# Kernel tuning notes

Hardware: AMD Instinct MI355X
Metric: run time of the kernel (lower is better)

The kernel has to match this reference:

```python
import jax, jax.numpy as jnp
import numpy as np

EPS = 1e-5
NUM_GROUPS = 8


def setup_inputs() -> dict:
    key = jax.random.key(0)
    ks = jax.random.split(key, 8)
    B, C, H, W = 4, 64, 64, 64
    scale_w = 1.0 / np.sqrt(C)  # roughly xavier scale for [C,C]
    return {
        "x": jax.random.normal(ks[0], (B, C, H, W), dtype=jnp.float32),
        "gamma": jnp.ones((C,), dtype=jnp.float32),
        "beta": jnp.zeros((C,), dtype=jnp.float32),
        "Wq": jax.random.normal(ks[1], (C, C), dtype=jnp.float32) * scale_w,
        "bq": jnp.zeros((C,), dtype=jnp.float32),
        "Wk": jax.random.normal(ks[2], (C, C), dtype=jnp.float32) * scale_w,
        "bk": jnp.zeros((C,), dtype=jnp.float32),
        "Wv": jax.random.normal(ks[3], (C, C), dtype=jnp.float32) * scale_w,
        "bv": jnp.zeros((C,), dtype=jnp.float32),
        "Wp": jax.random.normal(ks[4], (C, C), dtype=jnp.float32) * scale_w,
        "bp": jnp.zeros((C,), dtype=jnp.float32),
    }


def _group_norm(x, gamma, beta):
    # x: [B, C, H, W]; normalize over (C//G, H, W) within each of G groups
    B, C, H, W = x.shape
    xg = x.reshape(B, NUM_GROUPS, -1)
    mean = jnp.mean(xg, axis=-1, keepdims=True)
    var = jnp.var(xg, axis=-1, keepdims=True)
    xn = ((xg - mean) * jax.lax.rsqrt(var + EPS)).reshape(B, C, H, W)
    return xn * gamma[None, :, None, None] + beta[None, :, None, None]


def reference(x, gamma, beta, Wq, bq, Wk, bk, Wv, bv, Wp, bp):
    B, C, H, W = x.shape
    N = H * W
    xn = _group_norm(x, gamma, beta).reshape(B, C, N)  # [B, C, N]
    # 1x1 convs == per-pixel linear maps over channels
    q = jnp.einsum('oc,bcn->bon', Wq, xn) + bq[None, :, None]  # [B, C, N]
    k = jnp.einsum('oc,bcn->bon', Wk, xn) + bk[None, :, None]
    v = jnp.einsum('oc,bcn->bon', Wv, xn) + bv[None, :, None]
    scale = 1.0 / jnp.sqrt(jnp.asarray(C, dtype=x.dtype))
    attn = jnp.einsum('bcn,bcm->bnm', q, k) * scale  # [B, N, N]
    attn = jax.nn.softmax(attn, axis=-1)
    out = jnp.einsum('bnm,bcm->bcn', attn, v)  # [B, C, N]
    out = jnp.einsum('oc,bcn->bon', Wp, out) + bp[None, :, None]
    return x + out.reshape(B, C, H, W)
```

## Files before the change

kernel.cpp:

```cpp
#include <hip/hip_runtime.h>
#include <math.h>

#define B_ 4
#define C_ 64
#define N_ 4096

typedef unsigned short u16;
typedef __attribute__((ext_vector_type(8))) short bf16x8;
typedef __attribute__((ext_vector_type(4))) float f32x4;
typedef __attribute__((ext_vector_type(16))) float f32x16;
typedef __attribute__((ext_vector_type(2))) int i32x2;

__device__ __forceinline__ u16 f2bf(float f) {
    unsigned u = __float_as_uint(f);
    u += 0x7fff + ((u >> 16) & 1);
    return (u16)(u >> 16);
}
__device__ __forceinline__ float bf2f(u16 h) {
    return __uint_as_float(((unsigned)h) << 16);
}

__global__ __launch_bounds__(256) void gn_reduce(const float* __restrict__ x,
                                                 float* __restrict__ partials) {
    int bg = blockIdx.x >> 3, chunk = blockIdx.x & 7;
    const float4* xv = (const float4*)(x + (size_t)bg * 32768 + (size_t)chunk * 4096);
    float s = 0.f, ss = 0.f;
    #pragma unroll
    for (int k = 0; k < 4; k++) {
        float4 v = xv[threadIdx.x + 256 * k];
        s += v.x + v.y + v.z + v.w;
        ss += v.x * v.x + v.y * v.y + v.z * v.z + v.w * v.w;
    }
    #pragma unroll
    for (int off = 1; off < 64; off <<= 1) {
        s += __shfl_xor(s, off);
        ss += __shfl_xor(ss, off);
    }
    __shared__ float red[2][4];
    int w = threadIdx.x >> 6;
    if ((threadIdx.x & 63) == 0) { red[0][w] = s; red[1][w] = ss; }
    __syncthreads();
    if (threadIdx.x == 0) {
        s = red[0][0] + red[0][1] + red[0][2] + red[0][3];
        ss = red[1][0] + red[1][1] + red[1][2] + red[1][3];
        partials[bg * 16 + chunk * 2] = s;
        partials[bg * 16 + chunk * 2 + 1] = ss;
    }
}

__global__ __launch_bounds__(256) void qkv_kernel(
    const float* __restrict__ x, const float* __restrict__ gamma,
    const float* __restrict__ beta, const float* __restrict__ partials,
    const float* __restrict__ Wq, const float* __restrict__ bq,
    const float* __restrict__ Wk, const float* __restrict__ bk,
    const float* __restrict__ Wv, const float* __restrict__ bv,
    u16* __restrict__ Qo, u16* __restrict__ Ko, u16* __restrict__ Vt) {
    __shared__ __align__(16) u16 wt[3][64][64];
    __shared__ __align__(16) u16 xs[64][64];
    __shared__ __align__(16) u16 odt[64][72];

    const int b = blockIdx.x >> 6;
    const int nt = blockIdx.x & 63;
    const int tid = threadIdx.x;
    const float* Ws[3] = {Wq, Wk, Wv};
    const float* bs[3] = {bq, bk, bv};

    {
        const int rw = tid >> 2, qd = tid & 3;
        #pragma unroll
        for (int s = 0; s < 3; s++) {
            const float4* wsrc = (const float4*)(Ws[s] + rw * 64 + qd * 16);
            float4 f0 = wsrc[0], f1 = wsrc[1], f2 = wsrc[2], f3 = wsrc[3];
            u16 pk[16];
            pk[0]=f2bf(f0.x); pk[1]=f2bf(f0.y); pk[2]=f2bf(f0.z); pk[3]=f2bf(f0.w);
            pk[4]=f2bf(f1.x); pk[5]=f2bf(f1.y); pk[6]=f2bf(f1.z); pk[7]=f2bf(f1.w);
            pk[8]=f2bf(f2.x); pk[9]=f2bf(f2.y); pk[10]=f2bf(f2.z); pk[11]=f2bf(f2.w);
            pk[12]=f2bf(f3.x); pk[13]=f2bf(f3.y); pk[14]=f2bf(f3.z); pk[15]=f2bf(f3.w);
            int blk0 = (2 * qd) ^ (rw & 7), blk1 = (2 * qd + 1) ^ (rw & 7);
            *(uint4*)&wt[s][rw][blk0 * 8] = *(uint4*)&pk[0];
            *(uint4*)&wt[s][rw][blk1 * 8] = *(uint4*)&pk[8];
        }
    }
    {
        const int c = tid >> 2, px0 = (tid & 3) * 16;
        const int g = c >> 3, bg = b * 8 + g;
        float s = 0.f, ss = 0.f;
        #pragma unroll
        for (int i = 0; i < 8; i++) {
            s += partials[bg * 16 + i * 2];
            ss += partials[bg * 16 + i * 2 + 1];
        }
        float mean = s * (1.f / 32768.f);
        float var = ss * (1.f / 32768.f) - mean * mean;
        float rstd = rsqrtf(var + 1e-5f);
        float ga = gamma[c] * rstd;
        float bb = beta[c] - mean * ga;
        const float4* xp = (const float4*)(x + ((size_t)(b * 64 + c)) * N_ + nt * 64 + px0);
        float4 q0 = xp[0], q1 = xp[1], q2 = xp[2], q3 = xp[3];
        float vals[16] = {q0.x,q0.y,q0.z,q0.w, q1.x,q1.y,q1.z,q1.w,
                          q2.x,q2.y,q2.z,q2.w, q3.x,q3.y,q3.z,q3.w};
        #pragma unroll
        for (int e = 0; e < 16; e++) {
            int px = px0 + e;
            xs[px][((c >> 3) ^ (px & 7)) * 8 + (c & 7)] = f2bf(vals[e] * ga + bb);
        }
    }
    __syncthreads();

    const int lane = tid & 63, w = tid >> 6;
    const int lr = lane & 15, lg = lane >> 4;
    const f32x4 zz = {0.f, 0.f, 0.f, 0.f};
    const int sa0 = (lg ^ (lr & 7)) * 8, sa1 = ((4 | lg) ^ (lr & 7)) * 8;

    #pragma unroll
    for (int s = 0; s < 3; s++) {
        bf16x8 a0 = *(const bf16x8*)&wt[s][w * 16 + lr][sa0];
        bf16x8 a1 = *(const bf16x8*)&wt[s][w * 16 + lr][sa1];
        float bias[4];
        #pragma unroll
        for (int r = 0; r < 4; r++) bias[r] = bs[s][w * 16 + lg * 4 + r];
        #pragma unroll
        for (int pt = 0; pt < 4; pt++) {
            bf16x8 b0 = *(const bf16x8*)&xs[pt * 16 + lr][sa0];
            bf16x8 b1 = *(const bf16x8*)&xs[pt * 16 + lr][sa1];
            f32x4 acc = __builtin_amdgcn_mfma_f32_16x16x32_bf16(a0, b0, zz, 0, 0, 0);
            acc = __builtin_amdgcn_mfma_f32_16x16x32_bf16(a1, b1, acc, 0, 0, 0);
            if (s == 0) {
                #pragma unroll
                for (int r = 0; r < 4; r++)
                    odt[pt * 16 + lr][w * 16 + lg * 4 + r] = f2bf((acc[r] + bias[r]) * 0.18033688f);
            } else if (s == 1) {
                #pragma unroll
                for (int r = 0; r < 4; r++)
                    odt[pt * 16 + lr][w * 16 + lg * 4 + r] = f2bf(acc[r] + bias[r]);
            } else {
                #pragma unroll
                for (int r = 0; r < 4; r++)
                    odt[w * 16 + lg * 4 + r][pt * 16 + lr] = f2bf(acc[r] + bias[r]);
            }
        }
        __syncthreads();
        if (s < 2) {
            u16* dst = (s == 0 ? Qo : Ko) + ((size_t)(b * N_ + nt * 64)) * 64;
            #pragma unroll
            for (int k2 = 0; k2 < 2; k2++) {
                int c = tid + k2 * 256;
                int px = c >> 3, blk = c & 7;
                *(uint4*)(dst + (size_t)px * 64 + blk * 8) = *(const uint4*)&odt[px][blk * 8];
            }
        } else {
            #pragma unroll
            for (int k2 = 0; k2 < 2; k2++) {
                int c = tid + k2 * 256;
                int co = c >> 3, blk = c & 7;
                *(uint4*)(Vt + ((size_t)(b * 64 + co)) * N_ + nt * 64 + blk * 8) =
                    *(const uint4*)&odt[co][blk * 8];
            }
        }
        __syncthreads();
    }
}

__global__ __launch_bounds__(256, 4) void flash_kernel(
    const u16* __restrict__ Qg, const u16* __restrict__ Kg,
    const u16* __restrict__ Vg, u16* __restrict__ Opart, float* __restrict__ ml,
    int nsplit) {
    __shared__ __align__(16) u16 smem[16384];
    u16* const Ksb0 = smem;
    u16* const Ksb1 = smem + 4096;
    u16* const Vsb0 = smem + 8192;
    u16* const Vsb1 = smem + 12288;

    const int sp = blockIdx.x >> 8;
    const int b  = (blockIdx.x >> 6) & 3;
    const int qt = blockIdx.x & 63;
    const int tid = threadIdx.x;
    const int w = tid >> 6, lane = tid & 63;
    const int l31 = lane & 31, lh = lane >> 5;
    const int qh = w >> 1, kh = w & 1;

    const int per = (nsplit == 4) ? 16 : (nsplit == 3) ? 22 : 32;
    const int kt0 = sp * per;
    const int NT = min(per, 64 - kt0);

    const u16* qptr = Qg + ((size_t)(b * N_ + qt * 64 + qh * 32 + l31)) * 64 + lh * 8;
    bf16x8 q0 = *(const bf16x8*)(qptr);
    bf16x8 q1 = *(const bf16x8*)(qptr + 16);
    bf16x8 q2 = *(const bf16x8*)(qptr + 32);
    bf16x8 q3 = *(const bf16x8*)(qptr + 48);

    const int srow = tid >> 2;
    const int scb  = (tid & 3) * 32;
    const char* Kbase = (const char*)(Kg + (size_t)b * N_ * C_) + (size_t)srow * 128 + scb;
    const char* Vbase = (const char*)(Vg + (size_t)b * C_ * N_) + (size_t)srow * (N_ * 2) + scb;
    const int se0 = srow * 64 + (((scb)      ^ ((srow & 7) << 4)) >> 1);
    const int se1 = srow * 64 + (((scb + 16) ^ ((srow & 7) << 4)) >> 1);

    const int key = kh * 32 + l31;
    int kaoff[4];
    #pragma unroll
    for (int s = 0; s < 4; s++)
        kaoff[s] = key * 64 + (((s * 2 + lh) ^ (key & 7)) << 3);
    int vboff[2][2];
    #pragma unroll
    for (int c = 0; c < 2; c++) {
        int ch = c * 32 + l31;
        #pragma unroll
        for (int s = 0; s < 2; s++)
            vboff[c][s] = ch * 64 + (((kh * 4 + s * 2 + lh) ^ (ch & 7)) << 3);
    }

    {
        uint4 k0a = *(const uint4*)(Kbase + (size_t)kt0 * 8192);
        uint4 k0b = *(const uint4*)(Kbase + (size_t)kt0 * 8192 + 16);
        uint4 v0a = *(const uint4*)(Vbase + kt0 * 128);
        uint4 v0b = *(const uint4*)(Vbase + kt0 * 128 + 16);
        *(uint4*)&Ksb0[se0] = k0a;  *(uint4*)&Ksb0[se1] = k0b;
        *(uint4*)&Vsb0[se0] = v0a;  *(uint4*)&Vsb0[se1] = v0b;
    }
    uint4 ka = *(const uint4*)(Kbase + (size_t)(kt0 + 1) * 8192);
    uint4 kb = *(const uint4*)(Kbase + (size_t)(kt0 + 1) * 8192 + 16);
    uint4 va = *(const uint4*)(Vbase + (kt0 + 1) * 128);
    uint4 vb = *(const uint4*)(Vbase + (kt0 + 1) * 128 + 16);
    __syncthreads();

    f32x16 o0, o1;
    #pragma unroll
    for (int r = 0; r < 16; r++) { o0[r] = 0.f; o1[r] = 0.f; }
    float lsum = 0.f;

    auto body = [&](int t, int bi) {
        const u16* ks = bi ? Ksb1 : Ksb0;
        const u16* vs = bi ? Vsb1 : Vsb0;
        u16* kd = bi ? Ksb0 : Ksb1;
        u16* vd = bi ? Vsb0 : Vsb1;

        f32x16 st;
        #pragma unroll
        for (int r = 0; r < 16; r++) st[r] = 0.f;
        __builtin_amdgcn_s_setprio(1);
        st = __builtin_amdgcn_mfma_f32_32x32x16_bf16(*(const bf16x8*)&ks[kaoff[0]], q0, st, 0, 0, 0);
        st = __builtin_amdgcn_mfma_f32_32x32x16_bf16(*(const bf16x8*)&ks[kaoff[1]], q1, st, 0, 0, 0);
        st = __builtin_amdgcn_mfma_f32_32x32x16_bf16(*(const bf16x8*)&ks[kaoff[2]], q2, st, 0, 0, 0);
        st = __builtin_amdgcn_mfma_f32_32x32x16_bf16(*(const bf16x8*)&ks[kaoff[3]], q3, st, 0, 0, 0);
        __builtin_amdgcn_s_setprio(0);

        float p[16];
        #pragma unroll
        for (int r = 0; r < 16; r++) p[r] = exp2f(st[r] - 12.f);
        lsum += (((p[0]+p[1])+(p[2]+p[3])) + ((p[4]+p[5])+(p[6]+p[7])))
              + (((p[8]+p[9])+(p[10]+p[11])) + ((p[12]+p[13])+(p[14]+p[15])));

        unsigned c0,c1,c2,c3,c4,c5,c6,c7;
        asm("v_cvt_pk_bf16_f32 %0, %1, %2" : "=v"(c0) : "v"(p[0]),  "v"(p[1]));
        asm("v_cvt_pk_bf16_f32 %0, %1, %2" : "=v"(c1) : "v"(p[2]),  "v"(p[3]));
        asm("v_cvt_pk_bf16_f32 %0, %1, %2" : "=v"(c2) : "v"(p[4]),  "v"(p[5]));
        asm("v_cvt_pk_bf16_f32 %0, %1, %2" : "=v"(c3) : "v"(p[6]),  "v"(p[7]));
        asm("v_cvt_pk_bf16_f32 %0, %1, %2" : "=v"(c4) : "v"(p[8]),  "v"(p[9]));
        asm("v_cvt_pk_bf16_f32 %0, %1, %2" : "=v"(c5) : "v"(p[10]), "v"(p[11]));
        asm("v_cvt_pk_bf16_f32 %0, %1, %2" : "=v"(c6) : "v"(p[12]), "v"(p[13]));
        asm("v_cvt_pk_bf16_f32 %0, %1, %2" : "=v"(c7) : "v"(p[14]), "v"(p[15]));
        i32x2 r02 = __builtin_amdgcn_permlane32_swap((int)c0, (int)c2, false, false);
        i32x2 r13 = __builtin_amdgcn_permlane32_swap((int)c1, (int)c3, false, false);
        i32x2 r46 = __builtin_amdgcn_permlane32_swap((int)c4, (int)c6, false, false);
        i32x2 r57 = __builtin_amdgcn_permlane32_swap((int)c5, (int)c7, false, false);
        union U { int u[4]; bf16x8 v; };
        U pa0 = {{r02[0], r13[0], r02[1], r13[1]}};
        U pa1 = {{r46[0], r57[0], r46[1], r57[1]}};

        __builtin_amdgcn_s_setprio(1);
        o0 = __builtin_amdgcn_mfma_f32_32x32x16_bf16(pa0.v, *(const bf16x8*)&vs[vboff[0][0]], o0, 0, 0, 0);
        o0 = __builtin_amdgcn_mfma_f32_32x32x16_bf16(pa1.v, *(const bf16x8*)&vs[vboff[0][1]], o0, 0, 0, 0);
        o1 = __builtin_amdgcn_mfma_f32_32x32x16_bf16(pa0.v, *(const bf16x8*)&vs[vboff[1][0]], o1, 0, 0, 0);
        o1 = __builtin_amdgcn_mfma_f32_32x32x16_bf16(pa1.v, *(const bf16x8*)&vs[vboff[1][1]], o1, 0, 0, 0);
        __builtin_amdgcn_s_setprio(0);

        if (t < NT - 1) {
            *(uint4*)&kd[se0] = ka;  *(uint4*)&kd[se1] = kb;
            *(uint4*)&vd[se0] = va;  *(uint4*)&vd[se1] = vb;
        }
        __syncthreads();
        if (t < NT - 2) {
            int kt = kt0 + t + 2;
            ka = *(const uint4*)(Kbase + (size_t)kt * 8192);
            kb = *(const uint4*)(Kbase + (size_t)kt * 8192 + 16);
            va = *(const uint4*)(Vbase + kt * 128);
            vb = *(const uint4*)(Vbase + kt * 128 + 16);
        }
    };
    for (int tt = 0; tt < NT; tt += 2) { body(tt, 0); body(tt + 1, 1); }

    float* red = (float*)smem;
    u16* ost = smem + 10240;
    if (kh == 1) {
        float* dst = red + (qh * 64 + lane) * 34;
        #pragma unroll
        for (int r = 0; r < 16; r++) { dst[r] = o0[r]; dst[16 + r] = o1[r]; }
        dst[32] = lsum;
    }
    __syncthreads();
    if (kh == 0) {
        const float* src = red + (qh * 64 + lane) * 34;
        float l2 = lsum + src[32];
        i32x2 rr = __builtin_amdgcn_permlane32_swap(__float_as_int(l2), __float_as_int(l2), false, false);
        float lpart = __int_as_float(lh ? rr[0] : rr[1]);
        float lfull = l2 + lpart;
        #pragma unroll
        for (int r = 0; r < 16; r++) {
            float v0 = o0[r] + src[r];
            float v1 = o1[r] + src[16 + r];
            int ql = qh * 32 + (r & 3) + 8 * (r >> 2) + 4 * lh;
            ost[ql * 64 + l31] = f2bf(v0);
            ost[ql * 64 + 32 + l31] = f2bf(v1);
        }
        if (lane < 32)
            ml[(size_t)sp * 16384 + b * N_ + qt * 64 + qh * 32 + l31] = lfull;
    }
    __syncthreads();
    uint4* op = (uint4*)(Opart + (size_t)sp * 1048576 + ((size_t)(b * N_ + qt * 64)) * 64);
    const uint4* os4 = (const uint4*)ost;
    op[tid] = os4[tid];
    op[tid + 256] = os4[tid + 256];
}

__global__ __launch_bounds__(256) void proj_kernel(
    const u16* __restrict__ Opart, const float* __restrict__ ml,
    const float* __restrict__ Wp, const float* __restrict__ bp,
    const float* __restrict__ x, float* __restrict__ out, int nsplit) {
    __shared__ __align__(16) u16 wp[64][64];
    __shared__ __align__(16) u16 og[64][64];
    const int b = blockIdx.x >> 6;
    const int nt = blockIdx.x & 63;
    const int tid = threadIdx.x;

    {
        const int rw = tid >> 2, qd = tid & 3;
        const float4* wsrc = (const float4*)(Wp + rw * 64 + qd * 16);
        float4 f0 = wsrc[0], f1 = wsrc[1], f2 = wsrc[2], f3 = wsrc[3];
        u16 pk[16];
        pk[0]=f2bf(f0.x); pk[1]=f2bf(f0.y); pk[2]=f2bf(f0.z); pk[3]=f2bf(f0.w);
        pk[4]=f2bf(f1.x); pk[5]=f2bf(f1.y); pk[6]=f2bf(f1.z); pk[7]=f2bf(f1.w);
        pk[8]=f2bf(f2.x); pk[9]=f2bf(f2.y); pk[10]=f2bf(f2.z); pk[11]=f2bf(f2.w);
        pk[12]=f2bf(f3.x); pk[13]=f2bf(f3.y); pk[14]=f2bf(f3.z); pk[15]=f2bf(f3.w);
        int blk0 = (2 * qd) ^ (rw & 7), blk1 = (2 * qd + 1) ^ (rw & 7);
        *(uint4*)&wp[rw][blk0 * 8] = *(uint4*)&pk[0];
        *(uint4*)&wp[rw][blk1 * 8] = *(uint4*)&pk[8];
    }
    {
        #pragma unroll
        for (int k2 = 0; k2 < 2; k2++) {
            int cidx = tid + k2 * 256;
            int px = cidx >> 3, blk = cidx & 7;
            int gpix = b * N_ + nt * 64 + px;
            float lsum = 0.f;
            for (int s = 0; s < nsplit; s++) lsum += ml[(size_t)s * 16384 + gpix];
            float inv = 1.f / lsum;
            float acc8[8] = {0.f,0.f,0.f,0.f,0.f,0.f,0.f,0.f};
            for (int s = 0; s < nsplit; s++) {
                u16 ov[8];
                *(uint4*)ov = *(const uint4*)(Opart + (size_t)s * 1048576 + (size_t)gpix * 64 + blk * 8);
                #pragma unroll
                for (int j = 0; j < 8; j++) acc8[j] += bf2f(ov[j]);
            }
            u16 y[8];
            #pragma unroll
            for (int j = 0; j < 8; j++) y[j] = f2bf(acc8[j] * inv);
            *(uint4*)&og[px][(blk ^ (px & 7)) * 8] = *(uint4*)y;
        }
    }
    __syncthreads();

    const int lane = tid & 63, w = tid >> 6;
    const int lr = lane & 15, lg = lane >> 4;
    const f32x4 zz = {0.f, 0.f, 0.f, 0.f};
    const int sa0 = (lg ^ (lr & 7)) * 8, sa1 = ((4 | lg) ^ (lr & 7)) * 8;

    bf16x8 a0 = *(const bf16x8*)&wp[w * 16 + lr][sa0];
    bf16x8 a1 = *(const bf16x8*)&wp[w * 16 + lr][sa1];
    float bias[4];
    #pragma unroll
    for (int r = 0; r < 4; r++) bias[r] = bp[w * 16 + lg * 4 + r];

    #pragma unroll
    for (int pt = 0; pt < 4; pt++) {
        bf16x8 b0 = *(const bf16x8*)&og[pt * 16 + lr][sa0];
        bf16x8 b1 = *(const bf16x8*)&og[pt * 16 + lr][sa1];
        f32x4 acc = __builtin_amdgcn_mfma_f32_16x16x32_bf16(a0, b0, zz, 0, 0, 0);
        acc = __builtin_amdgcn_mfma_f32_16x16x32_bf16(a1, b1, acc, 0, 0, 0);
        #pragma unroll
        for (int r = 0; r < 4; r++) {
            int cout = w * 16 + lg * 4 + r;
            int px = pt * 16 + lr;
            size_t idx = ((size_t)(b * 64 + cout)) * N_ + nt * 64 + px;
            out[idx] = x[idx] + bias[r] + acc[r];
        }
    }
}

extern "C" void kernel_launch(void* const* d_in, const int* in_sizes, int n_in,
                              void* d_out, int out_size, void* d_ws, size_t ws_size,
                              hipStream_t stream) {
    const float* x     = (const float*)d_in[0];
    const float* gamma = (const float*)d_in[1];
    const float* beta  = (const float*)d_in[2];
    const float* Wq    = (const float*)d_in[3];
    const float* bq    = (const float*)d_in[4];
    const float* Wk    = (const float*)d_in[5];
    const float* bk    = (const float*)d_in[6];
    const float* Wv    = (const float*)d_in[7];
    const float* bv    = (const float*)d_in[8];
    const float* Wp    = (const float*)d_in[9];
    const float* bp    = (const float*)d_in[10];
    float* out = (float*)d_out;

    const size_t elems = (size_t)B_ * N_ * C_;
    const size_t base = 4096 + 262144;
    float* partials = (float*)d_ws;
    float* ml = (float*)((char*)d_ws + 4096);
    u16* Qb = (u16*)((char*)d_ws + base);
    u16* Kb = Qb + elems;
    u16* Vt = Kb + elems;
    u16* Opart = Vt + elems;

    const size_t need4 = base + 3 * elems * 2 + 4 * elems * 2;
    const size_t need3 = base + 3 * elems * 2 + 3 * elems * 2;
    const int nsplit = (ws_size >= need4) ? 4 : (ws_size >= need3) ? 3 : 2;

    gn_reduce<<<256, 256, 0, stream>>>(x, partials);
    qkv_kernel<<<256, 256, 0, stream>>>(x, gamma, beta, partials,
                                        Wq, bq, Wk, bk, Wv, bv, Qb, Kb, Vt);
    flash_kernel<<<nsplit * 256, 256, 0, stream>>>(Qb, Kb, Vt, Opart, ml, nsplit);
    proj_kernel<<<256, 256, 0, stream>>>(Opart, ml, Wp, bp, x, out, nsplit);
}
```

Measured before the change: 54.66 us.

## Software-pipeline PV MFMAs one iteration behind QK MFMAs in attention loop

Restructures the attention inner loop so each iteration's P·V MFMAs use the probabilities and V fragments from the previous tile. They are issued before the current tile's QK MFMAs, and V fragments are preloaded into registers before the barrier. The aim is to overlap the softmax exp/convert work with matrix-core work. In exchange it adds extra live registers and drops the manual two-iteration unroll, which may add buffer-select overhead or register pressure.

```diff
diff --git a/kernel.cpp b/kernel.cpp
--- a/kernel.cpp
+++ b/kernel.cpp
@@ -229,11 +229,29 @@
     for (int r = 0; r < 16; r++) { o0[r] = 0.f; o1[r] = 0.f; }
     float lsum = 0.f;
 
-    auto body = [&](int t, int bi) {
+    bf16x8 paC0 = {}, paC1 = {};
+    bf16x8 vC0 = {}, vC1 = {}, vC2 = {}, vC3 = {};
+
+    for (int t = 0; t < NT; ++t) {
+        const int bi = t & 1;
         const u16* ks = bi ? Ksb1 : Ksb0;
         const u16* vs = bi ? Vsb1 : Vsb0;
         u16* kd = bi ? Ksb0 : Ksb1;
         u16* vd = bi ? Vsb0 : Vsb1;
+
+        bf16x8 vN0 = *(const bf16x8*)&vs[vboff[0][0]];
+        bf16x8 vN1 = *(const bf16x8*)&vs[vboff[0][1]];
+        bf16x8 vN2 = *(const bf16x8*)&vs[vboff[1][0]];
+        bf16x8 vN3 = *(const bf16x8*)&vs[vboff[1][1]];
+
+        if (t > 0) {
+            __builtin_amdgcn_s_setprio(1);
+            o0 = __builtin_amdgcn_mfma_f32_32x32x16_bf16(paC0, vC0, o0, 0, 0, 0);
+            o0 = __builtin_amdgcn_mfma_f32_32x32x16_bf16(paC1, vC1, o0, 0, 0, 0);
+            o1 = __builtin_amdgcn_mfma_f32_32x32x16_bf16(paC0, vC2, o1, 0, 0, 0);
+            o1 = __builtin_amdgcn_mfma_f32_32x32x16_bf16(paC1, vC3, o1, 0, 0, 0);
+            __builtin_amdgcn_s_setprio(0);
+        }
 
         f32x16 st;
         #pragma unroll
@@ -245,21 +263,19 @@
         st = __builtin_amdgcn_mfma_f32_32x32x16_bf16(*(const bf16x8*)&ks[kaoff[3]], q3, st, 0, 0, 0);
         __builtin_amdgcn_s_setprio(0);
 
-        float p[16];
-        #pragma unroll
-        for (int r = 0; r < 16; r++) p[r] = exp2f(st[r] - 12.f);
-        lsum += (((p[0]+p[1])+(p[2]+p[3])) + ((p[4]+p[5])+(p[6]+p[7])))
-              + (((p[8]+p[9])+(p[10]+p[11])) + ((p[12]+p[13])+(p[14]+p[15])));
-
+        #pragma unroll
+        for (int r = 0; r < 16; r++) st[r] = exp2f(st[r] - 12.f);
+        lsum += (((st[0]+st[1])+(st[2]+st[3])) + ((st[4]+st[5])+(st[6]+st[7])))
+              + (((st[8]+st[9])+(st[10]+st[11])) + ((st[12]+st[13])+(st[14]+st[15])));
         unsigned c0,c1,c2,c3,c4,c5,c6,c7;
-        asm("v_cvt_pk_bf16_f32 %0, %1, %2" : "=v"(c0) : "v"(p[0]),  "v"(p[1]));
-        asm("v_cvt_pk_bf16_f32 %0, %1, %2" : "=v"(c1) : "v"(p[2]),  "v"(p[3]));
-        asm("v_cvt_pk_bf16_f32 %0, %1, %2" : "=v"(c2) : "v"(p[4]),  "v"(p[5]));
-        asm("v_cvt_pk_bf16_f32 %0, %1, %2" : "=v"(c3) : "v"(p[6]),  "v"(p[7]));
-        asm("v_cvt_pk_bf16_f32 %0, %1, %2" : "=v"(c4) : "v"(p[8]),  "v"(p[9]));
-        asm("v_cvt_pk_bf16_f32 %0, %1, %2" : "=v"(c5) : "v"(p[10]), "v"(p[11]));
-        asm("v_cvt_pk_bf16_f32 %0, %1, %2" : "=v"(c6) : "v"(p[12]), "v"(p[13]));
-        asm("v_cvt_pk_bf16_f32 %0, %1, %2" : "=v"(c7) : "v"(p[14]), "v"(p[15]));
+        asm("v_cvt_pk_bf16_f32 %0, %1, %2" : "=v"(c0) : "v"(st[0]),  "v"(st[1]));
+        asm("v_cvt_pk_bf16_f32 %0, %1, %2" : "=v"(c1) : "v"(st[2]),  "v"(st[3]));
+        asm("v_cvt_pk_bf16_f32 %0, %1, %2" : "=v"(c2) : "v"(st[4]),  "v"(st[5]));
+        asm("v_cvt_pk_bf16_f32 %0, %1, %2" : "=v"(c3) : "v"(st[6]),  "v"(st[7]));
+        asm("v_cvt_pk_bf16_f32 %0, %1, %2" : "=v"(c4) : "v"(st[8]),  "v"(st[9]));
+        asm("v_cvt_pk_bf16_f32 %0, %1, %2" : "=v"(c5) : "v"(st[10]), "v"(st[11]));
+        asm("v_cvt_pk_bf16_f32 %0, %1, %2" : "=v"(c6) : "v"(st[12]), "v"(st[13]));
+        asm("v_cvt_pk_bf16_f32 %0, %1, %2" : "=v"(c7) : "v"(st[14]), "v"(st[15]));
         i32x2 r02 = __builtin_amdgcn_permlane32_swap((int)c0, (int)c2, false, false);
         i32x2 r13 = __builtin_amdgcn_permlane32_swap((int)c1, (int)c3, false, false);
         i32x2 r46 = __builtin_amdgcn_permlane32_swap((int)c4, (int)c6, false, false);
@@ -267,13 +283,8 @@
         union U { int u[4]; bf16x8 v; };
         U pa0 = {{r02[0], r13[0], r02[1], r13[1]}};
         U pa1 = {{r46[0], r57[0], r46[1], r57[1]}};
-
-        __builtin_amdgcn_s_setprio(1);
-        o0 = __builtin_amdgcn_mfma_f32_32x32x16_bf16(pa0.v, *(const bf16x8*)&vs[vboff[0][0]], o0, 0, 0, 0);
-        o0 = __builtin_amdgcn_mfma_f32_32x32x16_bf16(pa1.v, *(const bf16x8*)&vs[vboff[0][1]], o0, 0, 0, 0);
-        o1 = __builtin_amdgcn_mfma_f32_32x32x16_bf16(pa0.v, *(const bf16x8*)&vs[vboff[1][0]], o1, 0, 0, 0);
-        o1 = __builtin_amdgcn_mfma_f32_32x32x16_bf16(pa1.v, *(const bf16x8*)&vs[vboff[1][1]], o1, 0, 0, 0);
-        __builtin_amdgcn_s_setprio(0);
+        paC0 = pa0.v;
+        paC1 = pa1.v;
 
         if (t < NT - 1) {
             *(uint4*)&kd[se0] = ka;  *(uint4*)&kd[se1] = kb;
@@ -287,8 +298,14 @@
             va = *(const uint4*)(Vbase + kt * 128);
             vb = *(const uint4*)(Vbase + kt * 128 + 16);
         }
-    };
-    for (int tt = 0; tt < NT; tt += 2) { body(tt, 0); body(tt + 1, 1); }
+
+        vC0 = vN0; vC1 = vN1; vC2 = vN2; vC3 = vN3;
+    }
+
+    o0 = __builtin_amdgcn_mfma_f32_32x32x16_bf16(paC0, vC0, o0, 0, 0, 0);
+    o0 = __builtin_amdgcn_mfma_f32_32x32x16_bf16(paC1, vC1, o0, 0, 0, 0);
+    o1 = __builtin_amdgcn_mfma_f32_32x32x16_bf16(paC0, vC2, o1, 0, 0, 0);
+    o1 = __builtin_amdgcn_mfma_f32_32x32x16_bf16(paC1, vC3, o1, 0, 0, 0);
 
     float* red = (float*)smem;
     u16* ost = smem + 10240;
```

Result: slower. 56.17 us (+2.8%).
